# Kernel tuning notes

Measured on AMD Instinct MI355X. Metric: run time of the kernel, lower is better.

## Reference

```python
import jax, jax.numpy as jnp
import numpy as np

D_MODEL = 64
N_HEADS = 4
HEAD_DIM = D_MODEL // N_HEADS
D_FF = 128
EPS = 1e-5


def _layernorm(x, gamma, beta):
    mu = jnp.mean(x, axis=-1, keepdims=True)
    var = jnp.mean(jnp.square(x - mu), axis=-1, keepdims=True)
    return (x - mu) * jax.lax.rsqrt(var + EPS) * gamma + beta


def setup_inputs() -> dict:
    key = jax.random.key(0)
    ks = jax.random.split(key, 8)
    b, t = 16, 2048
    s = 0.05  # weight init scale
    return {
        "x": jax.random.normal(ks[0], (b, t, D_MODEL), dtype=jnp.float32),
        "Wqkv": jax.random.normal(ks[1], (3 * D_MODEL, D_MODEL), dtype=jnp.float32) * s,
        "Wproj": jax.random.normal(ks[2], (D_MODEL, D_MODEL), dtype=jnp.float32) * s,
        "W1": jax.random.normal(ks[3], (D_FF, D_MODEL), dtype=jnp.float32) * s,
        "b1": jax.random.normal(ks[4], (D_FF,), dtype=jnp.float32) * s,
        "W2": jax.random.normal(ks[5], (D_MODEL, D_FF), dtype=jnp.float32) * s,
        "b2": jax.random.normal(ks[6], (D_MODEL,), dtype=jnp.float32) * s,
        "g1": jnp.ones((D_MODEL,), dtype=jnp.float32),
        "be1": jnp.zeros((D_MODEL,), dtype=jnp.float32),
        "g2": jnp.ones((D_MODEL,), dtype=jnp.float32),
        "be2": jnp.zeros((D_MODEL,), dtype=jnp.float32),
    }


def reference(x, Wqkv, Wproj, W1, b1, W2, b2, g1, be1, g2, be2):
    b, t, c = x.shape
    # qkv: [b,t,3c] -> [b,t,3,h,hd] -> unbind into q,k,v each [b,h,t,hd]
    qkv = jnp.einsum('btc,ec->bte', x, Wqkv)
    qkv = qkv.reshape(b, t, 3, N_HEADS, HEAD_DIM)
    q = jnp.transpose(qkv[:, :, 0], (0, 2, 1, 3))
    k = jnp.transpose(qkv[:, :, 1], (0, 2, 1, 3))
    v = jnp.transpose(qkv[:, :, 2], (0, 2, 1, 3))
    scale = HEAD_DIM ** -0.5
    attn = jnp.einsum('bhqd,bhkd->bhqk', q, k) * scale  # [b,h,t,t]
    attn = jax.nn.softmax(attn, axis=-1)
    a = jnp.einsum('bhqk,bhkd->bhqd', attn, v)          # [b,h,t,hd]
    a = jnp.transpose(a, (0, 2, 1, 3)).reshape(b, t, c)
    a = jnp.einsum('btc,dc->btd', a, Wproj)
    x = _layernorm(x + a, g1, be1)
    y = jnp.einsum('btc,fc->btf', x, W1) + b1
    y = jnp.einsum('btf,cf->btc', jax.nn.relu(y), W2) + b2
    return _layernorm(x + y, g2, be2)
```

## Files before the change

kernel.cpp:

```cpp
#include <hip/hip_runtime.h>
#include <hip/hip_bf16.h>
#include <math.h>

typedef _Float16 h16;
typedef h16   v4h __attribute__((ext_vector_type(4)));
typedef h16   h2  __attribute__((ext_vector_type(2)));
typedef float v4f __attribute__((ext_vector_type(4)));

#define T_SEQ 2048
#define BATCH 16
#define NTOK  (BATCH * T_SEQ)
#define C_DIM 64
#define N_H   4
#define HD    16
#define FF    128
#define EPS_LN 1e-5f
#define MFMA16 __builtin_amdgcn_mfma_f32_16x16x16f16
#define QSCALE (0.25f * 1.44269504089f * 1024.0f)
#define BMAGIC (12582912.0f + 15316.0f)

static __device__ __forceinline__ float frcp(float x) {
#if __has_builtin(__builtin_amdgcn_rcpf)
    return __builtin_amdgcn_rcpf(x);
#else
    return 1.0f / x;
#endif
}
static __device__ __forceinline__ float frsq(float x) {
#if __has_builtin(__builtin_amdgcn_rsqf)
    return __builtin_amdgcn_rsqf(x);
#else
    return rsqrtf(x);
#endif
}
static __device__ __forceinline__ float fdot2p(h2 a, float acc) {
#if __has_builtin(__builtin_amdgcn_fdot2)
    const h2 one2 = {(h16)1.0f, (h16)1.0f};
    return __builtin_amdgcn_fdot2(a, one2, acc, false);
#else
    return acc + (float)a[0] + (float)a[1];
#endif
}
static __device__ __forceinline__ v4h cvt4(v4f f) {
    v4h r; r[0]=(h16)f[0]; r[1]=(h16)f[1]; r[2]=(h16)f[2]; r[3]=(h16)f[3];
    return r;
}
static __device__ __forceinline__ h2 pkperm(float t0, float t1) {
    unsigned r = __builtin_amdgcn_perm(__builtin_bit_cast(unsigned, t1),
                                       __builtin_bit_cast(unsigned, t0),
                                       0x05040100u);
    return __builtin_bit_cast(h2, r);
}

__global__ __launch_bounds__(256) void prep_pack(
    const float* __restrict__ Wqkv, const float* __restrict__ Wproj,
    const float* __restrict__ W1,   const float* __restrict__ W2,
    v4h* __restrict__ wp)
{
    int fid = blockIdx.x * 256 + threadIdx.x;
    int lane = fid & 63;
    int lm = lane & 15, g4 = ((lane >> 4) & 3) * 4;
    int frag = fid >> 6;
    const float* src; int o, kt, K;
    if (fid < 3072)      { int f = frag;      o = f >> 2; kt = f & 3; K = 64;  src = Wqkv;  }
    else if (fid < 4096) { int f = frag - 48; o = f >> 2; kt = f & 3; K = 64;  src = Wproj; }
    else if (fid < 6144) { int f = frag - 64; o = f >> 2; kt = f & 3; K = 64;  src = W1;    }
    else                 { int f = frag - 96; o = f >> 3; kt = f & 7; K = 128; src = W2;    }
    v4f v = *(const v4f*)(src + (o*16 + lm)*K + kt*16 + g4);
    wp[fid] = cvt4(v);
}

__global__ __launch_bounds__(256) void qkv_gemm(
    const float* __restrict__ x, const v4h* __restrict__ wq,
    h16* __restrict__ q, h16* __restrict__ k, h16* __restrict__ vt)
{
    int tid = threadIdx.x;
    int lane = tid & 63, w = tid >> 6;
    int lm = lane & 15, g4 = (lane >> 4) * 4;
    int tile = blockIdx.x;
    int t0 = tile * 16;
    int ng = w;

    __shared__ h16 xs[16][72];
    {
        v4f v = *(const v4f*)(x + (size_t)t0 * C_DIM + tid * 4);
        int r = tid >> 4;
        int c = (tid & 15) * 4;
        *(v4h*)&xs[r][c] = cvt4(v);
    }
    __syncthreads();

    v4h af[4];
#pragma unroll
    for (int kt = 0; kt < 4; kt++)
        af[kt] = *(const v4h*)&xs[lm][kt*16 + g4];

    int b = t0 >> 11, tl = t0 & (T_SEQ - 1);
#pragma unroll
    for (int j = 0; j < 3; j++) {
        int n = ng * 3 + j;
        v4f acc = {0.f, 0.f, 0.f, 0.f};
#pragma unroll
        for (int kt = 0; kt < 4; kt++)
            acc = MFMA16(af[kt], wq[(n*4 + kt)*64 + lane], acc, 0, 0, 0);
        if (n < 4) {
            h16* qp = q + ((size_t)(b*N_H + n)*T_SEQ + tl + g4)*HD + lm;
#pragma unroll
            for (int r = 0; r < 4; r++) qp[r*HD] = (h16)(acc[r] * QSCALE);
        } else if (n < 8) {
            h16* kp = k + ((size_t)(b*N_H + (n-4))*T_SEQ + tl + g4)*HD + lm;
#pragma unroll
            for (int r = 0; r < 4; r++) kp[r*HD] = (h16)acc[r];
        } else {
            v4h pk;
#pragma unroll
            for (int r = 0; r < 4; r++) pk[r] = (h16)acc[r];
            *(v4h*)(vt + ((size_t)(b*N_H + (n-8))*(T_SEQ/16) + (tl >> 4))*256
                       + lm*16 + g4) = pk;
        }
    }
}

__global__ __launch_bounds__(256, 2) void attn_mfma(
    const h16* __restrict__ q, const h16* __restrict__ k,
    const h16* __restrict__ vt, h16* __restrict__ a)
{
    int tid = threadIdx.x;
    int lane = tid & 63, w = tid >> 6;
    int lm = lane & 15, g4 = (lane >> 4) * 4;
    int bid = blockIdx.x;
    int W = (bid & 7) * 64 + (bid >> 3);
    int bh = W >> 3;
    int q256 = W & 7;
    int q0 = q256 * 256 + (w & 1) * 128;
    int khalf = w >> 1;

    v4h qf[8];
#pragma unroll
    for (int j = 0; j < 8; j++)
        qf[j] = *(const v4h*)(q + ((size_t)bh*T_SEQ + q0 + j*16 + lm)*HD + g4);
    const h16* kpl = k  + ((size_t)bh*T_SEQ + khalf*1024 + lm)*HD + g4;
    const h16* vpl = vt + ((size_t)bh*(T_SEQ/16) + khalf*64)*256 + lm*16 + g4;

    v4f acc[8] = {{0,0,0,0},{0,0,0,0},{0,0,0,0},{0,0,0,0},
                  {0,0,0,0},{0,0,0,0},{0,0,0,0},{0,0,0,0}};
    float l[8] = {0.f,0.f,0.f,0.f,0.f,0.f,0.f,0.f};
    const v4f bvec = {BMAGIC, BMAGIC, BMAGIC, BMAGIC};

    for (int kt = 0; kt < 16; kt++) {
        v4h kf[4], vf[4];
#pragma unroll
        for (int m = 0; m < 4; m++) {
            kf[m] = *(const v4h*)(kpl + m*256);
            vf[m] = *(const v4h*)(vpl + m*256);
        }
        kpl += 1024; vpl += 1024;
        __builtin_amdgcn_sched_barrier(0);
#pragma unroll
        for (int m = 0; m < 4; m++) {
#pragma unroll
            for (int j = 0; j < 8; j++) {
                v4f t = MFMA16(kf[m], qf[j], bvec, 0, 0, 0);
                h2 a0 = pkperm(t[0], t[1]);
                h2 b0 = pkperm(t[2], t[3]);
                l[j] = fdot2p(a0, l[j]);
                l[j] = fdot2p(b0, l[j]);
                v4h p = __builtin_shufflevector(a0, b0, 0, 1, 2, 3);
                acc[j] = MFMA16(vf[m], p, acc[j], 0, 0, 0);
            }
        }
    }

#pragma unroll
    for (int j = 0; j < 8; j++) {
        float lj = l[j];
        lj += __shfl_xor(lj, 16, 64); lj += __shfl_xor(lj, 32, 64);
        l[j] = lj;
    }

    __shared__ float lds[2][64][41];
    if (w >= 2) {
        float* p = lds[w - 2][lane];
#pragma unroll
        for (int j = 0; j < 8; j++) {
            p[j] = l[j];
#pragma unroll
            for (int r = 0; r < 4; r++) p[8 + j*4 + r] = acc[j][r];
        }
    }
    __syncthreads();
    if (w < 2) {
        const float* p = lds[w][lane];
        int b = bh >> 2, h = bh & 3;
#pragma unroll
        for (int j = 0; j < 8; j++) {
            float inv = frcp(l[j] + p[j]);
            v4h o;
#pragma unroll
            for (int r = 0; r < 4; r++)
                o[r] = (h16)((acc[j][r] + p[8 + j*4 + r]) * inv);
            *(v4h*)(a + ((size_t)(b*T_SEQ) + q0 + j*16 + lm)*C_DIM + h*HD + g4) = o;
        }
    }
}

__global__ __launch_bounds__(256) void tail_fused(
    const h16* __restrict__ a, const float* __restrict__ x,
    const v4h* __restrict__ wp,
    const float* __restrict__ b1, const float* __restrict__ b2,
    const float* __restrict__ g1, const float* __restrict__ be1,
    const float* __restrict__ g2, const float* __restrict__ be2,
    float* __restrict__ out)
{
    int tid = threadIdx.x;
    int lane = tid & 63, w = tid >> 6;
    int lm = lane & 15, g4 = (lane >> 4) * 4;
    int pair = w >> 1;
    int half = w & 1;
    int t0 = (blockIdx.x * 2 + pair) * 16;

    const v4h* whp = wp + 3072;
    const v4h* wh1 = wp + 4096;
    const v4h* wh2 = wp + 6144;

    v4h af[4];
#pragma unroll
    for (int kt = 0; kt < 4; kt++)
        af[kt] = *(const v4h*)(a + (size_t)(t0 + lm)*C_DIM + kt*16 + g4);

    float rvn[4][4];
    v4h x1t[4];
    {
        v4h wf[16];
#pragma unroll
        for (int f = 0; f < 16; f++) wf[f] = whp[f*64 + lane];
        __builtin_amdgcn_sched_barrier(0);
        v4f rv[4];
#pragma unroll
        for (int cn = 0; cn < 4; cn++) {
            v4f acc = {0.f, 0.f, 0.f, 0.f};
#pragma unroll
            for (int kt = 0; kt < 4; kt++)
                acc = MFMA16(wf[cn*4 + kt], af[kt], acc, 0, 0, 0);
            v4f xr = *(const v4f*)(x + (size_t)(t0 + lm)*C_DIM + cn*16 + g4);
            rv[cn] = acc + xr;
        }
        float s = 0.f;
#pragma unroll
        for (int cn = 0; cn < 4; cn++)
#pragma unroll
            for (int i = 0; i < 4; i++) s += rv[cn][i];
        s += __shfl_xor(s, 16, 64); s += __shfl_xor(s, 32, 64);
        float mu = s * (1.f/64.f);
        float qs = 0.f;
#pragma unroll
        for (int cn = 0; cn < 4; cn++)
#pragma unroll
            for (int i = 0; i < 4; i++) { float d = rv[cn][i] - mu; qs += d*d; }
        qs += __shfl_xor(qs, 16, 64); qs += __shfl_xor(qs, 32, 64);
        float is = frsq(qs * (1.f/64.f) + EPS_LN);
#pragma unroll
        for (int cn = 0; cn < 4; cn++) {
            v4f g1v = *(const v4f*)(g1 + cn*16 + g4);
            v4f bev = *(const v4f*)(be1 + cn*16 + g4);
#pragma unroll
            for (int i = 0; i < 4; i++) {
                float vl = (rv[cn][i] - mu) * is * g1v[i] + bev[i];
                rvn[cn][i] = vl;
                x1t[cn][i] = (h16)vl;
            }
        }
    }
    __builtin_amdgcn_sched_barrier(0);

    v4h ht[4];
    {
        v4h wf[16];
#pragma unroll
        for (int f = 0; f < 16; f++) wf[f] = wh1[(half*16 + f)*64 + lane];
        __builtin_amdgcn_sched_barrier(0);
#pragma unroll
        for (int j = 0; j < 4; j++) {
            int nf = half * 4 + j;
            v4f acc = {0.f, 0.f, 0.f, 0.f};
#pragma unroll
            for (int kt = 0; kt < 4; kt++)
                acc = MFMA16(wf[j*4 + kt], x1t[kt], acc, 0, 0, 0);
            v4f b1v = *(const v4f*)(b1 + nf*16 + g4);
#pragma unroll
            for (int i = 0; i < 4; i++) ht[j][i] = (h16)fmaxf(acc[i] + b1v[i], 0.f);
        }
    }
    __builtin_amdgcn_sched_barrier(0);

    float yp[4][4];
    {
        v4h wf[16];
#pragma unroll
        for (int cn = 0; cn < 4; cn++)
#pragma unroll
            for (int j = 0; j < 4; j++)
                wf[cn*4 + j] = wh2[(cn*8 + half*4 + j)*64 + lane];
        __builtin_amdgcn_sched_barrier(0);
#pragma unroll
        for (int cn = 0; cn < 4; cn++) {
            v4f acc = {0.f, 0.f, 0.f, 0.f};
#pragma unroll
            for (int j = 0; j < 4; j++)
                acc = MFMA16(wf[cn*4 + j], ht[j], acc, 0, 0, 0);
#pragma unroll
            for (int i = 0; i < 4; i++) yp[cn][i] = acc[i];
        }
    }

    __shared__ float lds[2][64][17];
    if (half == 1) {
        float* p = lds[pair][lane];
#pragma unroll
        for (int cn = 0; cn < 4; cn++)
#pragma unroll
            for (int i = 0; i < 4; i++) p[cn*4 + i] = yp[cn][i];
    }
    __syncthreads();
    if (half == 0) {
        const float* p = lds[pair][lane];
        float yv[4][4];
#pragma unroll
        for (int cn = 0; cn < 4; cn++) {
            v4f b2v = *(const v4f*)(b2 + cn*16 + g4);
#pragma unroll
            for (int i = 0; i < 4; i++)
                yv[cn][i] = yp[cn][i] + p[cn*4 + i] + b2v[i] + rvn[cn][i];
        }
        float s2 = 0.f;
#pragma unroll
        for (int cn = 0; cn < 4; cn++)
#pragma unroll
            for (int i = 0; i < 4; i++) s2 += yv[cn][i];
        s2 += __shfl_xor(s2, 16, 64); s2 += __shfl_xor(s2, 32, 64);
        float mu2 = s2 * (1.f/64.f);
        float qs2 = 0.f;
#pragma unroll
        for (int cn = 0; cn < 4; cn++)
#pragma unroll
            for (int i = 0; i < 4; i++) { float d = yv[cn][i] - mu2; qs2 += d*d; }
        qs2 += __shfl_xor(qs2, 16, 64); qs2 += __shfl_xor(qs2, 32, 64);
        float is2 = frsq(qs2 * (1.f/64.f) + EPS_LN);
#pragma unroll
        for (int cn = 0; cn < 4; cn++) {
            v4f g2v = *(const v4f*)(g2 + cn*16 + g4);
            v4f bev = *(const v4f*)(be2 + cn*16 + g4);
            v4f o;
#pragma unroll
            for (int i = 0; i < 4; i++) o[i] = (yv[cn][i] - mu2) * is2 * g2v[i] + bev[i];
            *(v4f*)(out + (size_t)(t0 + lm)*C_DIM + cn*16 + g4) = o;
        }
    }
}

extern "C" void kernel_launch(void* const* d_in, const int* in_sizes, int n_in,
                              void* d_out, int out_size, void* d_ws, size_t ws_size,
                              hipStream_t stream)
{
    const float* x     = (const float*)d_in[0];
    const float* Wqkv  = (const float*)d_in[1];
    const float* Wproj = (const float*)d_in[2];
    const float* W1    = (const float*)d_in[3];
    const float* b1    = (const float*)d_in[4];
    const float* W2    = (const float*)d_in[5];
    const float* b2    = (const float*)d_in[6];
    const float* g1    = (const float*)d_in[7];
    const float* be1   = (const float*)d_in[8];
    const float* g2    = (const float*)d_in[9];
    const float* be2   = (const float*)d_in[10];
    float* out = (float*)d_out;

    const size_t perQ = (size_t)BATCH * N_H * T_SEQ * HD;
    h16* q   = (h16*)d_ws;
    h16* kk  = q  + perQ;
    h16* vt  = kk + perQ;
    h16* a   = vt + perQ;
    v4h* wp  = (v4h*)(a + (size_t)NTOK * C_DIM);

    prep_pack  <<<32,   256, 0, stream>>>(Wqkv, Wproj, W1, W2, wp);
    qkv_gemm   <<<2048, 256, 0, stream>>>(x, wp, q, kk, vt);
    attn_mfma  <<<512,  256, 0, stream>>>(q, kk, vt, a);
    tail_fused <<<1024, 256, 0, stream>>>(a, x, wp, b1, b2,
                                          g1, be1, g2, be2, out);
}
```

Before: 62.88 us.

## Split attention keys four ways per block with each wave covering all 256 queries

Each of the four waves in an attention block now processes all 256 query rows of the block over a quarter of the keys (512), instead of 128 queries over half the keys. This halves how often each K/V fragment is reloaded per query tile and doubles the MFMA work per K/V load. The cost is double the register footprint for Q fragments and accumulators (16 tiles), which may pressure occupancy at launch_bounds(256,2). It also brings a larger LDS reduction in which three waves write partials and only wave 0 combines and stores, serialising the epilogue.

```diff
diff --git a/kernel.cpp b/kernel.cpp
--- a/kernel.cpp
+++ b/kernel.cpp
@@ -132,22 +132,25 @@
     int W = (bid & 7) * 64 + (bid >> 3);
     int bh = W >> 3;
     int q256 = W & 7;
-    int q0 = q256 * 256 + (w & 1) * 128;
-    int khalf = w >> 1;
-
-    v4h qf[8];
-#pragma unroll
-    for (int j = 0; j < 8; j++)
+    int q0 = q256 * 256;
+    int kq = w;
+
+    v4h qf[16];
+#pragma unroll
+    for (int j = 0; j < 16; j++)
         qf[j] = *(const v4h*)(q + ((size_t)bh*T_SEQ + q0 + j*16 + lm)*HD + g4);
-    const h16* kpl = k  + ((size_t)bh*T_SEQ + khalf*1024 + lm)*HD + g4;
-    const h16* vpl = vt + ((size_t)bh*(T_SEQ/16) + khalf*64)*256 + lm*16 + g4;
-
-    v4f acc[8] = {{0,0,0,0},{0,0,0,0},{0,0,0,0},{0,0,0,0},
-                  {0,0,0,0},{0,0,0,0},{0,0,0,0},{0,0,0,0}};
-    float l[8] = {0.f,0.f,0.f,0.f,0.f,0.f,0.f,0.f};
+    const h16* kpl = k  + ((size_t)bh*T_SEQ + kq*512 + lm)*HD + g4;
+    const h16* vpl = vt + ((size_t)bh*(T_SEQ/16) + kq*32)*256 + lm*16 + g4;
+
+    v4f acc[16];
+#pragma unroll
+    for (int j = 0; j < 16; j++) acc[j] = (v4f){0.f, 0.f, 0.f, 0.f};
+    float l[16];
+#pragma unroll
+    for (int j = 0; j < 16; j++) l[j] = 0.f;
     const v4f bvec = {BMAGIC, BMAGIC, BMAGIC, BMAGIC};
 
-    for (int kt = 0; kt < 16; kt++) {
+    for (int kt = 0; kt < 8; kt++) {
         v4h kf[4], vf[4];
 #pragma unroll
         for (int m = 0; m < 4; m++) {
@@ -159,7 +162,7 @@
 #pragma unroll
         for (int m = 0; m < 4; m++) {
 #pragma unroll
-            for (int j = 0; j < 8; j++) {
+            for (int j = 0; j < 16; j++) {
                 v4f t = MFMA16(kf[m], qf[j], bvec, 0, 0, 0);
                 h2 a0 = pkperm(t[0], t[1]);
                 h2 b0 = pkperm(t[2], t[3]);
@@ -172,33 +175,37 @@
     }
 
 #pragma unroll
-    for (int j = 0; j < 8; j++) {
+    for (int j = 0; j < 16; j++) {
         float lj = l[j];
         lj += __shfl_xor(lj, 16, 64); lj += __shfl_xor(lj, 32, 64);
         l[j] = lj;
     }
 
-    __shared__ float lds[2][64][41];
-    if (w >= 2) {
-        float* p = lds[w - 2][lane];
-#pragma unroll
-        for (int j = 0; j < 8; j++) {
+    __shared__ float lds[3][64][81];
+    if (w >= 1) {
+        float* p = lds[w - 1][lane];
+#pragma unroll
+        for (int j = 0; j < 16; j++) {
             p[j] = l[j];
 #pragma unroll
-            for (int r = 0; r < 4; r++) p[8 + j*4 + r] = acc[j][r];
+            for (int r = 0; r < 4; r++) p[16 + j*4 + r] = acc[j][r];
         }
     }
     __syncthreads();
-    if (w < 2) {
-        const float* p = lds[w][lane];
+    if (w == 0) {
         int b = bh >> 2, h = bh & 3;
 #pragma unroll
-        for (int j = 0; j < 8; j++) {
-            float inv = frcp(l[j] + p[j]);
+        for (int j = 0; j < 16; j++) {
+            float lt = l[j] + lds[0][lane][j] + lds[1][lane][j] + lds[2][lane][j];
+            float inv = frcp(lt);
             v4h o;
 #pragma unroll
-            for (int r = 0; r < 4; r++)
-                o[r] = (h16)((acc[j][r] + p[8 + j*4 + r]) * inv);
+            for (int r = 0; r < 4; r++) {
+                float av = acc[j][r] + lds[0][lane][16 + j*4 + r]
+                                     + lds[1][lane][16 + j*4 + r]
+                                     + lds[2][lane][16 + j*4 + r];
+                o[r] = (h16)(av * inv);
+            }
             *(v4h*)(a + ((size_t)(b*T_SEQ) + q0 + j*16 + lm)*C_DIM + h*HD + g4) = o;
         }
     }
```

Result: slower. 66.37 us (+5.5%).
